# Optimization experiments

Measured on AMD Instinct MI355X. Metric: run time of the kernel, lower is better.

## Reference

```python
import jax, jax.numpy as jnp
import numpy as np

NUM_HEAD = 32
NUM_KV_HEAD = 8
HEAD_DIM = 128
EMBED_DIM = 4096
GROUP = NUM_HEAD // NUM_KV_HEAD + 2  # 6: 4 q slots + 1 k + 1 v
TOKENS = 64


def setup_inputs() -> dict:
    key = jax.random.key(0)
    k1, k2, k3 = jax.random.split(key, 3)
    inp = jax.random.normal(k1, (TOKENS, EMBED_DIM), dtype=jnp.float32)
    # fused GQA weight layout from load_parameter: [embed_dim, num_kv_head, group, head_dim]
    weight = jax.random.normal(k2, (EMBED_DIM, NUM_KV_HEAD, GROUP, HEAD_DIM), dtype=jnp.float32) * 0.02
    bias = jax.random.normal(k3, (NUM_KV_HEAD, GROUP, HEAD_DIM), dtype=jnp.float32) * 0.02
    return {"input": inp, "weight": weight, "bias": bias}


def reference(input, weight, bias):
    # fused grouped QKV GEMM (mm_qkv_group_out):
    # out[t, kv, g, d] = sum_e input[t, e] * weight[e, kv, g, d] + bias[kv, g, d]
    out = jnp.einsum('te,ekgd->tkgd', input, weight) + bias
    T = input.shape[0]
    q = out[:, :, : GROUP - 2, :].reshape(T, NUM_HEAD * HEAD_DIM)
    k = out[:, :, GROUP - 2, :].reshape(T, NUM_KV_HEAD * HEAD_DIM)
    v = out[:, :, GROUP - 1, :].reshape(T, NUM_KV_HEAD * HEAD_DIM)
    return (q, k, v)
```

## Files before the change

### kernel.cpp

```cpp
#include <hip/hip_runtime.h>


#define N_COLS 6144
#define K_DIM  4096
#define Q_SZ   (64 * 4096)
#define K_OFF  Q_SZ
#define V_OFF  (Q_SZ + 64 * 1024)
#define OUT_ELEMS 393216
#define NT     192
#define KSPLIT 4
#define BK     64
#define TILES  16

typedef __bf16 bf16x8 __attribute__((ext_vector_type(8)));
typedef float  f32x4  __attribute__((ext_vector_type(4)));

__device__ __forceinline__ int out_index(int t, int n) {
    const int kv = n / 768;
    const int g  = (n >> 7) % 6;
    const int d  = n & 127;
    if (g < 4)  return t * 4096 + kv * 512 + g * 128 + d;
    if (g == 4) return K_OFF + t * 1024 + kv * 128 + d;
    return V_OFF + t * 1024 + kv * 128 + d;
}

__global__ __launch_bounds__(256, 3)
void qkv_gemm(const float* __restrict__ in, const float* __restrict__ w,
              float* __restrict__ part) {
    __shared__ float Ws[2][BK * 32];

    const int tid  = threadIdx.x;
    const int nt   = blockIdx.x % NT;
    const int kq   = blockIdx.x / NT;
    const int n0   = nt * 32;
    const int k0   = kq * (BK * TILES);
    const int wid  = tid >> 6;
    const int lane = tid & 63;
    const int l15  = lane & 15;
    const int kblk = lane >> 4;

    const int t3 = tid >> 3;
    const int c  = tid & 7;

    f32x4 acc[2];
    acc[0] = (f32x4){0.f, 0.f, 0.f, 0.f};
    acc[1] = (f32x4){0.f, 0.f, 0.f, 0.f};

    f32x4 wreg[2][2];
    float4 a[4];

    const float* wbase = w + (size_t)k0 * N_COLS + n0 + c * 4;
    const float* abase = in + (size_t)(wid * 16 + l15) * K_DIM + k0 + kblk * 8;

    auto WLOAD = [&](int s, int set) {
        const float* p = wbase + (size_t)s * BK * N_COLS;
        #pragma unroll
        for (int r = 0; r < 2; ++r)
            wreg[set][r] = *(const f32x4*)(p + (size_t)(r * 32 + t3) * N_COLS);
    };
    auto DSWRITE = [&](int set, int buf) {
        #pragma unroll
        for (int r = 0; r < 2; ++r) {
            const int k  = r * 32 + t3;
            const int cc = c ^ (((k >> 3) & 1) << 2);
            *(f32x4*)&Ws[buf][k * 32 + 4 * cc] = wreg[set][r];
        }
    };
    auto ALOAD = [&](int s) {
        const float* ap = abase + (size_t)s * BK;
        a[0] = *(const float4*)ap;
        a[1] = *(const float4*)(ap + 4);
        a[2] = *(const float4*)(ap + 32);
        a[3] = *(const float4*)(ap + 36);
    };

    WLOAD(0, 0);
    ALOAD(0);
    WLOAD(1, 1);
    DSWRITE(0, 0);
    asm volatile("s_waitcnt lgkmcnt(0)" ::: "memory");
    __builtin_amdgcn_s_barrier();

    #pragma unroll
    for (int s = 0; s < TILES; ++s) {
        bf16x8 av[2];
        #pragma unroll
        for (int h = 0; h < 2; ++h) {
            av[h][0] = (__bf16)a[2*h].x;   av[h][1] = (__bf16)a[2*h].y;
            av[h][2] = (__bf16)a[2*h].z;   av[h][3] = (__bf16)a[2*h].w;
            av[h][4] = (__bf16)a[2*h+1].x; av[h][5] = (__bf16)a[2*h+1].y;
            av[h][6] = (__bf16)a[2*h+1].z; av[h][7] = (__bf16)a[2*h+1].w;
        }

        if (s + 2 < TILES) WLOAD(s + 2, s & 1);
        if (s + 1 < TILES) ALOAD(s + 1);

        #pragma unroll
        for (int h = 0; h < 2; ++h) {
            #pragma unroll
            for (int nfi = 0; nfi < 2; ++nfi) {
                const int nb   = nfi * 16 + l15;
                const int base = (h * 32 + kblk * 8) * 32 + (nb ^ ((kblk & 1) << 4));
                bf16x8 bv;
                #pragma unroll
                for (int j = 0; j < 8; ++j)
                    bv[j] = (__bf16)Ws[s & 1][base + j * 32];
                acc[nfi] = __builtin_amdgcn_mfma_f32_16x16x32_bf16(
                    av[h], bv, acc[nfi], 0, 0, 0);
            }
        }

        if (s + 1 < TILES) {
            DSWRITE((s + 1) & 1, (s + 1) & 1);
            asm volatile("s_waitcnt lgkmcnt(0)" ::: "memory");
            __builtin_amdgcn_s_barrier();
        }
    }

    float* pb = part + (size_t)kq * OUT_ELEMS;
    #pragma unroll
    for (int nfi = 0; nfi < 2; ++nfi) {
        const int n = n0 + nfi * 16 + l15;
        #pragma unroll
        for (int r = 0; r < 4; ++r) {
            const int t = wid * 16 + kblk * 4 + r;
            pb[(size_t)t * N_COLS + n] = acc[nfi][r];
        }
    }
}

__global__ __launch_bounds__(256)
void qkv_reduce(const float* __restrict__ part, const float* __restrict__ bias,
                float* __restrict__ out) {
    const int nt = blockIdx.x % NT;
    const int h  = blockIdx.x / NT;
    const int t  = h * 32 + (threadIdx.x >> 3);
    const int n  = nt * 32 + (threadIdx.x & 7) * 4;
    const size_t i = (size_t)t * N_COLS + n;
    f32x4 s = *(const f32x4*)(bias + n);
    #pragma unroll
    for (int kq = 0; kq < KSPLIT; ++kq)
        s += *(const f32x4*)(part + (size_t)kq * OUT_ELEMS + i);
    *(f32x4*)(out + out_index(t, n)) = s;
}

extern "C" void kernel_launch(void* const* d_in, const int* in_sizes, int n_in,
                              void* d_out, int out_size, void* d_ws, size_t ws_size,
                              hipStream_t stream) {
    const float* in   = (const float*)d_in[0];
    const float* w    = (const float*)d_in[1];
    const float* bias = (const float*)d_in[2];
    float* out  = (float*)d_out;
    float* part = (float*)d_ws;

    qkv_gemm<<<NT * KSPLIT, 256, 0, stream>>>(in, w, part);
    qkv_reduce<<<NT * 2, 256, 0, stream>>>(part, bias, out);
}
```

Baseline: 161.5 us.

## Drop split-K and reduce kernel; use 256 narrow 24-column tiles with fused bias

Removes the split-K partial-sum buffer and the separate reduction kernel. Each of 256 blocks now covers the full K range for a 24-column strip, so the grid matches the CU count, and bias plus the QKV scatter are applied directly in the epilogue. Weight loads use a deeper 3-stage register prefetch with BK=128. In exchange, each block runs a much longer serial K loop at occupancy 1, and one MFMA column block is only half used, which wastes some compute.

```diff
diff --git a/kernel.cpp b/kernel.cpp
--- a/kernel.cpp
+++ b/kernel.cpp
@@ -6,11 +6,10 @@
 #define Q_SZ   (64 * 4096)
 #define K_OFF  Q_SZ
 #define V_OFF  (Q_SZ + 64 * 1024)
-#define OUT_ELEMS 393216
-#define NT     192
-#define KSPLIT 4
-#define BK     64
-#define TILES  16
+#define NTW    24
+#define BK     128
+#define TILES  32
+#define LDSROW 24
 
 typedef __bf16 bf16x8 __attribute__((ext_vector_type(8)));
 typedef float  f32x4  __attribute__((ext_vector_type(4)));
@@ -24,124 +23,124 @@
     return V_OFF + t * 1024 + kv * 128 + d;
 }
 
-__global__ __launch_bounds__(256, 3)
+__global__ __launch_bounds__(256, 1)
 void qkv_gemm(const float* __restrict__ in, const float* __restrict__ w,
-              float* __restrict__ part) {
-    __shared__ float Ws[2][BK * 32];
+              const float* __restrict__ bias, float* __restrict__ out) {
+    __shared__ float Ws[2][BK * LDSROW + 16];
 
     const int tid  = threadIdx.x;
-    const int nt   = blockIdx.x % NT;
-    const int kq   = blockIdx.x / NT;
-    const int n0   = nt * 32;
-    const int k0   = kq * (BK * TILES);
+    const int nt   = ((int)blockIdx.x & 7) * 32 + ((int)blockIdx.x >> 3);
+    const int n0   = nt * NTW;
     const int wid  = tid >> 6;
     const int lane = tid & 63;
     const int l15  = lane & 15;
     const int kblk = lane >> 4;
 
-    const int t3 = tid >> 3;
-    const int c  = tid & 7;
+    int srow[3], scc[3];
+    #pragma unroll
+    for (int r = 0; r < 3; ++r) {
+        const int u = r * 256 + tid;
+        srow[r] = u / 6;
+        scc[r]  = u - srow[r] * 6;
+    }
 
     f32x4 acc[2];
     acc[0] = (f32x4){0.f, 0.f, 0.f, 0.f};
     acc[1] = (f32x4){0.f, 0.f, 0.f, 0.f};
 
-    f32x4 wreg[2][2];
-    float4 a[4];
+    f32x4 wreg[4][3];
+    float4 a[8];
 
-    const float* wbase = w + (size_t)k0 * N_COLS + n0 + c * 4;
-    const float* abase = in + (size_t)(wid * 16 + l15) * K_DIM + k0 + kblk * 8;
+    const float* wbase = w + n0;
+    const float* abase = in + (size_t)(wid * 16 + l15) * K_DIM + kblk * 8;
 
     auto WLOAD = [&](int s, int set) {
         const float* p = wbase + (size_t)s * BK * N_COLS;
         #pragma unroll
-        for (int r = 0; r < 2; ++r)
-            wreg[set][r] = *(const f32x4*)(p + (size_t)(r * 32 + t3) * N_COLS);
+        for (int r = 0; r < 3; ++r)
+            wreg[set][r] =
+                *(const f32x4*)(p + (size_t)srow[r] * N_COLS + scc[r] * 4);
     };
     auto DSWRITE = [&](int set, int buf) {
         #pragma unroll
-        for (int r = 0; r < 2; ++r) {
-            const int k  = r * 32 + t3;
-            const int cc = c ^ (((k >> 3) & 1) << 2);
-            *(f32x4*)&Ws[buf][k * 32 + 4 * cc] = wreg[set][r];
-        }
+        for (int r = 0; r < 3; ++r)
+            *(f32x4*)&Ws[buf][srow[r] * LDSROW + scc[r] * 4] = wreg[set][r];
     };
     auto ALOAD = [&](int s) {
         const float* ap = abase + (size_t)s * BK;
-        a[0] = *(const float4*)ap;
-        a[1] = *(const float4*)(ap + 4);
-        a[2] = *(const float4*)(ap + 32);
-        a[3] = *(const float4*)(ap + 36);
+        #pragma unroll
+        for (int q = 0; q < 4; ++q) {
+            a[2 * q]     = *(const float4*)(ap + q * 32);
+            a[2 * q + 1] = *(const float4*)(ap + q * 32 + 4);
+        }
+    };
+
+    auto STEP = [&](int s, int p, int set) {
+        bf16x8 av[4];
+        #pragma unroll
+        for (int q = 0; q < 4; ++q) {
+            av[q][0] = (__bf16)a[2*q].x;   av[q][1] = (__bf16)a[2*q].y;
+            av[q][2] = (__bf16)a[2*q].z;   av[q][3] = (__bf16)a[2*q].w;
+            av[q][4] = (__bf16)a[2*q+1].x; av[q][5] = (__bf16)a[2*q+1].y;
+            av[q][6] = (__bf16)a[2*q+1].z; av[q][7] = (__bf16)a[2*q+1].w;
+        }
+        if (s + 3 < TILES) WLOAD(s + 3, (set + 3) & 3);
+        if (s + 1 < TILES) ALOAD(s + 1);
+
+        #pragma unroll
+        for (int q = 0; q < 4; ++q) {
+            #pragma unroll
+            for (int nfi = 0; nfi < 2; ++nfi) {
+                const int nb = nfi * 16 + l15;
+                bf16x8 bv;
+                #pragma unroll
+                for (int j = 0; j < 8; ++j)
+                    bv[j] = (__bf16)Ws[p][(q * 32 + kblk * 8 + j) * LDSROW + nb];
+                acc[nfi] = __builtin_amdgcn_mfma_f32_16x16x32_bf16(
+                    av[q], bv, acc[nfi], 0, 0, 0);
+            }
+        }
+
+        if (s + 1 < TILES) {
+            DSWRITE((set + 1) & 3, p ^ 1);
+            asm volatile("s_waitcnt lgkmcnt(0)" ::: "memory");
+            __builtin_amdgcn_s_barrier();
+        }
     };
 
     WLOAD(0, 0);
     ALOAD(0);
     WLOAD(1, 1);
+    WLOAD(2, 2);
     DSWRITE(0, 0);
     asm volatile("s_waitcnt lgkmcnt(0)" ::: "memory");
     __builtin_amdgcn_s_barrier();
 
-    #pragma unroll
-    for (int s = 0; s < TILES; ++s) {
-        bf16x8 av[2];
-        #pragma unroll
-        for (int h = 0; h < 2; ++h) {
-            av[h][0] = (__bf16)a[2*h].x;   av[h][1] = (__bf16)a[2*h].y;
-            av[h][2] = (__bf16)a[2*h].z;   av[h][3] = (__bf16)a[2*h].w;
-            av[h][4] = (__bf16)a[2*h+1].x; av[h][5] = (__bf16)a[2*h+1].y;
-            av[h][6] = (__bf16)a[2*h+1].z; av[h][7] = (__bf16)a[2*h+1].w;
-        }
-
-        if (s + 2 < TILES) WLOAD(s + 2, s & 1);
-        if (s + 1 < TILES) ALOAD(s + 1);
-
-        #pragma unroll
-        for (int h = 0; h < 2; ++h) {
-            #pragma unroll
-            for (int nfi = 0; nfi < 2; ++nfi) {
-                const int nb   = nfi * 16 + l15;
-                const int base = (h * 32 + kblk * 8) * 32 + (nb ^ ((kblk & 1) << 4));
-                bf16x8 bv;
-                #pragma unroll
-                for (int j = 0; j < 8; ++j)
-                    bv[j] = (__bf16)Ws[s & 1][base + j * 32];
-                acc[nfi] = __builtin_amdgcn_mfma_f32_16x16x32_bf16(
-                    av[h], bv, acc[nfi], 0, 0, 0);
-            }
-        }
-
-        if (s + 1 < TILES) {
-            DSWRITE((s + 1) & 1, (s + 1) & 1);
-            asm volatile("s_waitcnt lgkmcnt(0)" ::: "memory");
-            __builtin_amdgcn_s_barrier();
-        }
+    for (int ss = 0; ss < TILES; ss += 4) {
+        STEP(ss + 0, 0, 0);
+        STEP(ss + 1, 1, 1);
+        STEP(ss + 2, 0, 2);
+        STEP(ss + 3, 1, 3);
     }
 
-    float* pb = part + (size_t)kq * OUT_ELEMS;
-    #pragma unroll
-    for (int nfi = 0; nfi < 2; ++nfi) {
-        const int n = n0 + nfi * 16 + l15;
+    {
+        const int n = n0 + l15;
+        const float b0 = bias[n];
         #pragma unroll
         for (int r = 0; r < 4; ++r) {
             const int t = wid * 16 + kblk * 4 + r;
-            pb[(size_t)t * N_COLS + n] = acc[nfi][r];
+            out[out_index(t, n)] = acc[0][r] + b0;
         }
     }
-}
-
-__global__ __launch_bounds__(256)
-void qkv_reduce(const float* __restrict__ part, const float* __restrict__ bias,
-                float* __restrict__ out) {
-    const int nt = blockIdx.x % NT;
-    const int h  = blockIdx.x / NT;
-    const int t  = h * 32 + (threadIdx.x >> 3);
-    const int n  = nt * 32 + (threadIdx.x & 7) * 4;
-    const size_t i = (size_t)t * N_COLS + n;
-    f32x4 s = *(const f32x4*)(bias + n);
-    #pragma unroll
-    for (int kq = 0; kq < KSPLIT; ++kq)
-        s += *(const f32x4*)(part + (size_t)kq * OUT_ELEMS + i);
-    *(f32x4*)(out + out_index(t, n)) = s;
+    if (l15 < 8) {
+        const int n = n0 + 16 + l15;
+        const float b1 = bias[n];
+        #pragma unroll
+        for (int r = 0; r < 4; ++r) {
+            const int t = wid * 16 + kblk * 4 + r;
+            out[out_index(t, n)] = acc[1][r] + b1;
+        }
+    }
 }
 
 extern "C" void kernel_launch(void* const* d_in, const int* in_sizes, int n_in,
@@ -151,8 +150,7 @@
     const float* w    = (const float*)d_in[1];
     const float* bias = (const float*)d_in[2];
     float* out  = (float*)d_out;
-    float* part = (float*)d_ws;
+    (void)d_ws; (void)ws_size;
 
-    qkv_gemm<<<NT * KSPLIT, 256, 0, stream>>>(in, w, part);
-    qkv_reduce<<<NT * 2, 256, 0, stream>>>(part, bias, out);
+    qkv_gemm<<<256, 256, 0, stream>>>(in, w, bias, out);
 }
```

After: 174.2 us. 1.08x slower.
